# Kernel tuning notes

Measured on AMD Instinct MI355X. Metric: run time of the kernel, lower is better.

The kernel has to match this reference:

```python
import jax, jax.numpy as jnp
import numpy as np

N_EMBED = 16384
CODE_DIM = 32

def l2norm(t, eps=1e-12):
    return t / jnp.clip(jnp.linalg.norm(t, axis=-1, keepdims=True), eps)

def setup_inputs() -> dict:
    key = jax.random.key(0)
    k1, k2 = jax.random.split(key)
    z = jax.random.normal(k1, (8, 1024, CODE_DIM), dtype=jnp.float32)
    codebook = l2norm(jax.random.normal(k2, (N_EMBED, CODE_DIM), dtype=jnp.float32))
    return {"z": z, "codebook": codebook}

def reference(z, codebook):
    # z: [B, S, D]; codebook: [N, D]
    zn = l2norm(z)
    zf = zn.reshape(-1, zn.shape[-1])  # [B*S, D]
    d = (jnp.sum(zf * zf, axis=1, keepdims=True)
         + jnp.sum(codebook * codebook, axis=1)
         - 2.0 * jnp.einsum('bd,nd->bn', zf, codebook))  # [B*S, N]
    encoding_indices = jnp.argmin(d, axis=1)  # [B*S]
    z_q = codebook[encoding_indices]  # [B*S, D]
    return z_q, encoding_indices
```

## Files before the change

### kernel.cpp

```cpp
#include <hip/hip_runtime.h>
#include <math.h>

#define M_ROWS   8192
#define N_CODES  16384
#define D_DIM    32
#define NTHREADS 256

#define DELTA_MARGIN  8e-5f

#define NCHUNK       16
#define CHUNK_CODES  (N_CODES / NCHUNK)
#define SCAN_SLOTS   256

typedef short bf16x8 __attribute__((ext_vector_type(8)));
typedef float f32x4  __attribute__((ext_vector_type(4)));

__device__ inline unsigned short bf16_rne(float f) {
    unsigned u = __float_as_uint(f);
    unsigned r = u + 0x7FFFu + ((u >> 16) & 1u);
    return (unsigned short)(r >> 16);
}

__device__ inline void pack_pair(float f0, float f1, unsigned& hi, unsigned& lo) {
    unsigned short h0 = bf16_rne(f0), h1 = bf16_rne(f1);
    float r0 = f0 - __uint_as_float((unsigned)h0 << 16);
    float r1 = f1 - __uint_as_float((unsigned)h1 << 16);
    unsigned short l0 = bf16_rne(r0), l1 = bf16_rne(r1);
    hi = (unsigned)h0 | ((unsigned)h1 << 16);
    lo = (unsigned)l0 | ((unsigned)l1 << 16);
}

__device__ inline unsigned sortable_u32(float f) {
    unsigned u = __float_as_uint(f);
    return (u & 0x80000000u) ? ~u : (u | 0x80000000u);
}

__global__ void vq_prep_pack(const float* __restrict__ z,
                             const float* __restrict__ codebook,
                             float* __restrict__ zn, float* __restrict__ zz,
                             float* __restrict__ cc,
                             unsigned* __restrict__ chi, unsigned* __restrict__ clo,
                             unsigned* __restrict__ zhi, unsigned* __restrict__ zlo,
                             int* __restrict__ todo_cnt) {
    int gid  = blockIdx.x * NTHREADS + threadIdx.x;
    int row  = gid >> 2;
    int part = gid & 3;
    if (gid == 0) *todo_cnt = 0;

    if (row < N_CODES) {
        const float4* r4 = reinterpret_cast<const float4*>(codebook + (size_t)row * D_DIM);
        float4 v[8];
#pragma unroll
        for (int h = 0; h < 8; ++h) v[h] = r4[h];
        float s = 0.f;
#pragma unroll
        for (int h = 0; h < 8; ++h) {
            s = fmaf(v[h].x, v[h].x, s);
            s = fmaf(v[h].y, v[h].y, s);
            s = fmaf(v[h].z, v[h].z, s);
            s = fmaf(v[h].w, v[h].w, s);
        }
        if (part == 0) cc[row] = s;
#pragma unroll
        for (int k = 0; k < 2; ++k) {
            int h = part * 2 + k;
            unsigned hi0, lo0, hi1, lo1;
            pack_pair(v[h].x, v[h].y, hi0, lo0);
            pack_pair(v[h].z, v[h].w, hi1, lo1);
            chi[row * 16 + 2 * h]     = hi0;  clo[row * 16 + 2 * h]     = lo0;
            chi[row * 16 + 2 * h + 1] = hi1;  clo[row * 16 + 2 * h + 1] = lo1;
        }
    } else {
        int r = row - N_CODES;
        const float4* r4 = reinterpret_cast<const float4*>(z + (size_t)r * D_DIM);
        float4 v[8];
#pragma unroll
        for (int h = 0; h < 8; ++h) v[h] = r4[h];
        float s = 0.f;
#pragma unroll
        for (int h = 0; h < 8; ++h) {
            s = fmaf(v[h].x, v[h].x, s);
            s = fmaf(v[h].y, v[h].y, s);
            s = fmaf(v[h].z, v[h].z, s);
            s = fmaf(v[h].w, v[h].w, s);
        }
        float norm = sqrtf(s);
        norm = fmaxf(norm, 1e-12f);
        float zs = 0.f;
        float4 w[8];
#pragma unroll
        for (int h = 0; h < 8; ++h) {
            w[h].x = v[h].x / norm;
            w[h].y = v[h].y / norm;
            w[h].z = v[h].z / norm;
            w[h].w = v[h].w / norm;
            zs = fmaf(w[h].x, w[h].x, zs);
            zs = fmaf(w[h].y, w[h].y, zs);
            zs = fmaf(w[h].z, w[h].z, zs);
            zs = fmaf(w[h].w, w[h].w, zs);
        }
        if (part == 0) zz[r] = zs;
        float4* zn4 = reinterpret_cast<float4*>(zn + (size_t)r * D_DIM);
#pragma unroll
        for (int k = 0; k < 2; ++k) {
            int h = part * 2 + k;
            zn4[h] = w[h];
            unsigned hi0, lo0, hi1, lo1;
            pack_pair(w[h].x, w[h].y, hi0, lo0);
            pack_pair(w[h].z, w[h].w, hi1, lo1);
            zhi[r * 16 + 2 * h]     = hi0;  zlo[r * 16 + 2 * h]     = lo0;
            zhi[r * 16 + 2 * h + 1] = hi1;  zlo[r * 16 + 2 * h + 1] = lo1;
        }
    }
}

template <int NS>
__global__ __launch_bounds__(NTHREADS, 4)
void vq_mfma(const unsigned short* __restrict__ zhi,
             const unsigned short* __restrict__ zlo,
             const unsigned short* __restrict__ chi,
             const unsigned short* __restrict__ clo,
             float* __restrict__ pmax1, float* __restrict__ pmax2,
             int* __restrict__ pidx) {
    constexpr int SLICE_CODES = N_CODES / NS;
    constexpr int NPAIR = SLICE_CODES / 32;

    const int tid  = threadIdx.x;
    const int wave = tid >> 6;
    const int lane = tid & 63;
    const int rb    = blockIdx.x & 63;
    const int slice = blockIdx.x >> 6;

    const int row_w = rb * 128 + wave * 32;
    const int l15 = lane & 15;
    const int kg  = lane >> 4;
    const int kc  = kg * 8;

    const bf16x8 a_hi0 = *reinterpret_cast<const bf16x8*>(zhi + (size_t)(row_w + l15) * 32 + kc);
    const bf16x8 a_lo0 = *reinterpret_cast<const bf16x8*>(zlo + (size_t)(row_w + l15) * 32 + kc);
    const bf16x8 a_hi1 = *reinterpret_cast<const bf16x8*>(zhi + (size_t)(row_w + 16 + l15) * 32 + kc);
    const bf16x8 a_lo1 = *reinterpret_cast<const bf16x8*>(zlo + (size_t)(row_w + 16 + l15) * 32 + kc);

    const f32x4 zero4 = {0.f, 0.f, 0.f, 0.f};

    float max1[8], max2[8];
    int   idx1[8];
#pragma unroll
    for (int q = 0; q < 8; ++q) { max1[q] = -3.4e38f; max2[q] = -3.4e38f; idx1[q] = 0x7FFFFFFF; }

    auto argup = [&](const f32x4& accA, const f32x4& accB, int code) {
#pragma unroll
        for (int e = 0; e < 4; ++e) {
            float s0 = accA[e];
            max2[e] = __builtin_amdgcn_fmed3f(s0, max1[e], max2[e]);
            bool gt0 = s0 > max1[e];
            max1[e] = gt0 ? s0 : max1[e];
            idx1[e] = gt0 ? code : idx1[e];

            float s1 = accB[e];
            max2[4 + e] = __builtin_amdgcn_fmed3f(s1, max1[4 + e], max2[4 + e]);
            bool gt1 = s1 > max1[4 + e];
            max1[4 + e] = gt1 ? s1 : max1[4 + e];
            idx1[4 + e] = gt1 ? code : idx1[4 + e];
        }
    };
    auto pair_compute = [&](const bf16x8& b0h, const bf16x8& b0l,
                            const bf16x8& b1h, const bf16x8& b1l, int code) {
        f32x4 a00 = __builtin_amdgcn_mfma_f32_16x16x32_bf16(a_lo0, b0l, zero4, 0, 0, 0);
        f32x4 a01 = __builtin_amdgcn_mfma_f32_16x16x32_bf16(a_lo1, b0l, zero4, 0, 0, 0);
        f32x4 a10 = __builtin_amdgcn_mfma_f32_16x16x32_bf16(a_lo0, b1l, zero4, 0, 0, 0);
        f32x4 a11 = __builtin_amdgcn_mfma_f32_16x16x32_bf16(a_lo1, b1l, zero4, 0, 0, 0);
        a00 = __builtin_amdgcn_mfma_f32_16x16x32_bf16(a_lo0, b0h, a00, 0, 0, 0);
        a01 = __builtin_amdgcn_mfma_f32_16x16x32_bf16(a_lo1, b0h, a01, 0, 0, 0);
        a10 = __builtin_amdgcn_mfma_f32_16x16x32_bf16(a_lo0, b1h, a10, 0, 0, 0);
        a11 = __builtin_amdgcn_mfma_f32_16x16x32_bf16(a_lo1, b1h, a11, 0, 0, 0);
        a00 = __builtin_amdgcn_mfma_f32_16x16x32_bf16(a_hi0, b0l, a00, 0, 0, 0);
        a01 = __builtin_amdgcn_mfma_f32_16x16x32_bf16(a_hi1, b0l, a01, 0, 0, 0);
        a10 = __builtin_amdgcn_mfma_f32_16x16x32_bf16(a_hi0, b1l, a10, 0, 0, 0);
        a11 = __builtin_amdgcn_mfma_f32_16x16x32_bf16(a_hi1, b1l, a11, 0, 0, 0);
        a00 = __builtin_amdgcn_mfma_f32_16x16x32_bf16(a_hi0, b0h, a00, 0, 0, 0);
        a01 = __builtin_amdgcn_mfma_f32_16x16x32_bf16(a_hi1, b0h, a01, 0, 0, 0);
        a10 = __builtin_amdgcn_mfma_f32_16x16x32_bf16(a_hi0, b1h, a10, 0, 0, 0);
        a11 = __builtin_amdgcn_mfma_f32_16x16x32_bf16(a_hi1, b1h, a11, 0, 0, 0);
        argup(a00, a01, code);
        argup(a10, a11, code + 16);
    };

    int code = slice * SLICE_CODES + l15;
    bf16x8 b0h = *reinterpret_cast<const bf16x8*>(chi + (size_t)code * 32 + kc);
    bf16x8 b0l = *reinterpret_cast<const bf16x8*>(clo + (size_t)code * 32 + kc);
    bf16x8 b1h = *reinterpret_cast<const bf16x8*>(chi + (size_t)(code + 16) * 32 + kc);
    bf16x8 b1l = *reinterpret_cast<const bf16x8*>(clo + (size_t)(code + 16) * 32 + kc);

    for (int p = 0; p < NPAIR - 1; ++p) {
        const int ncode = code + 32;
        const bf16x8 nb0h = *reinterpret_cast<const bf16x8*>(chi + (size_t)ncode * 32 + kc);
        const bf16x8 nb0l = *reinterpret_cast<const bf16x8*>(clo + (size_t)ncode * 32 + kc);
        const bf16x8 nb1h = *reinterpret_cast<const bf16x8*>(chi + (size_t)(ncode + 16) * 32 + kc);
        const bf16x8 nb1l = *reinterpret_cast<const bf16x8*>(clo + (size_t)(ncode + 16) * 32 + kc);

        pair_compute(b0h, b0l, b1h, b1l, code);

        b0h = nb0h; b0l = nb0l; b1h = nb1h; b1l = nb1l; code = ncode;
    }
    pair_compute(b0h, b0l, b1h, b1l, code);

#pragma unroll
    for (int q = 0; q < 8; ++q) {
        float m1 = max1[q], m2 = max2[q];
        int   i1 = idx1[q];
#pragma unroll
        for (int off = 1; off < 16; off <<= 1) {
            float o1 = __shfl_xor(m1, off);
            float o2 = __shfl_xor(m2, off);
            int   oi = __shfl_xor(i1, off);
            float nm2 = fmaxf(fminf(m1, o1), fmaxf(m2, o2));
            if (o1 > m1 || (o1 == m1 && oi < i1)) { m1 = o1; i1 = oi; }
            m2 = nm2;
        }
        max1[q] = m1; max2[q] = m2; idx1[q] = i1;
    }
    if (l15 == 0) {
#pragma unroll
        for (int q = 0; q < 8; ++q) {
            const int rt = q >> 2, e = q & 3;
            const int row = row_w + rt * 16 + kg * 4 + e;
            pmax1[slice * M_ROWS + row] = max1[q];
            pmax2[slice * M_ROWS + row] = max2[q];
            pidx [slice * M_ROWS + row] = idx1[q];
        }
    }
}

template <int NS>
__global__ void vq_merge(const float* __restrict__ codebook,
                         const float* __restrict__ pmax1,
                         const float* __restrict__ pmax2,
                         const int* __restrict__ pidx,
                         float* __restrict__ zq, float* __restrict__ idx_out,
                         int* __restrict__ todo_cnt, int* __restrict__ todo,
                         unsigned long long* __restrict__ rbest) {
    const int row = blockIdx.x * NTHREADS + threadIdx.x;
    float m1 = pmax1[row], m2 = pmax2[row];
    int   i1 = pidx[row];
#pragma unroll
    for (int s = 1; s < NS; ++s) {
        float o1 = pmax1[s * M_ROWS + row];
        float o2 = pmax2[s * M_ROWS + row];
        int   oi = pidx [s * M_ROWS + row];
        float nm2 = fmaxf(fminf(m1, o1), fmaxf(m2, o2));
        if (o1 > m1) { m1 = o1; i1 = oi; }
        m2 = nm2;
    }
    if (2.0f * (m1 - m2) > DELTA_MARGIN) {
        idx_out[row] = (float)i1;
        const float4* src = reinterpret_cast<const float4*>(codebook + (size_t)i1 * D_DIM);
        float4* dst = reinterpret_cast<float4*>(zq + (size_t)row * D_DIM);
#pragma unroll
        for (int k = 0; k < 8; ++k) dst[k] = src[k];
    } else {
        rbest[row] = 0xFFFFFFFFFFFFFFFFull;
        int p = atomicAdd(todo_cnt, 1);
        todo[p] = row;
    }
}

__global__ __launch_bounds__(NTHREADS)
void vq_cleanup_scan(const float* __restrict__ zn, const float* __restrict__ zz,
                     const float* __restrict__ codebook, const float* __restrict__ cc,
                     const int* __restrict__ todo_cnt, const int* __restrict__ todo,
                     unsigned long long* __restrict__ rbest) {
    const int n = *todo_cnt;
    const int chunk = blockIdx.x & (NCHUNK - 1);
    const int slot  = blockIdx.x >> 4;
    const int tid   = threadIdx.x;
    const int cbase = chunk * CHUNK_CODES;

    for (int i = slot; i < n; i += SCAN_SLOTS) {
        const int row = todo[i];

        float zr[D_DIM];
#pragma unroll
        for (int d = 0; d < D_DIM; ++d) zr[d] = zn[(size_t)row * D_DIM + d];
        const float zzv = zz[row];

        unsigned long long best = 0xFFFFFFFFFFFFFFFFull;
#pragma unroll
        for (int k = 0; k < CHUNK_CODES / NTHREADS; ++k) {
            const int c = cbase + tid + (k << 8);
            const float4* cb = reinterpret_cast<const float4*>(codebook + (size_t)c * D_DIM);
            float dot = 0.f;
#pragma unroll
            for (int h = 0; h < 8; ++h) {
                float4 v = cb[h];
                dot = fmaf(zr[4 * h + 0], v.x, dot);
                dot = fmaf(zr[4 * h + 1], v.y, dot);
                dot = fmaf(zr[4 * h + 2], v.z, dot);
                dot = fmaf(zr[4 * h + 3], v.w, dot);
            }
            float t = zzv + cc[c];
            float dist = fmaf(-2.f, dot, t);
            unsigned long long key =
                ((unsigned long long)sortable_u32(dist) << 32) | (unsigned)c;
            best = (key < best) ? key : best;
        }

#pragma unroll
        for (int off = 32; off >= 1; off >>= 1) {
            unsigned long long ob = __shfl_xor(best, off);
            best = (ob < best) ? ob : best;
        }
        if ((tid & 63) == 0) {
            atomicMin(&rbest[row], best);
        }
    }
}

__global__ __launch_bounds__(NTHREADS)
void vq_cleanup_final(const float* __restrict__ codebook,
                      const int* __restrict__ todo_cnt, const int* __restrict__ todo,
                      const unsigned long long* __restrict__ rbest,
                      float* __restrict__ zq, float* __restrict__ idx_out) {
    const int n = *todo_cnt;
    for (int i = blockIdx.x * NTHREADS + threadIdx.x; i < n; i += gridDim.x * NTHREADS) {
        const int row = todo[i];
        const int bi = (int)(unsigned)(rbest[row] & 0xFFFFFFFFull);
        idx_out[row] = (float)bi;
        const float4* src = reinterpret_cast<const float4*>(codebook + (size_t)bi * D_DIM);
        float4* dst = reinterpret_cast<float4*>(zq + (size_t)row * D_DIM);
#pragma unroll
        for (int k = 0; k < 8; ++k) dst[k] = src[k];
    }
}

#define R_TILE   32
#define NSLICE_F 4
#define SLICE_CODES_F (N_CODES / NSLICE_F)
#define C_TILE   256
#define N_TILES_F (SLICE_CODES_F / C_TILE)
#define CB_PAD   36

__global__ void vq_prep_basic(const float* __restrict__ z,
                              const float* __restrict__ codebook,
                              float* __restrict__ zn,
                              float* __restrict__ zz,
                              float* __restrict__ cc) {
    int gid = blockIdx.x * NTHREADS + threadIdx.x;
    if (blockIdx.x < 64) {
        const float* row = codebook + (size_t)gid * D_DIM;
        float s = 0.f;
#pragma unroll
        for (int d = 0; d < D_DIM; ++d) s = fmaf(row[d], row[d], s);
        cc[gid] = s;
    } else {
        int r = gid - N_CODES;
        const float* row = z + (size_t)r * D_DIM;
        float s = 0.f;
#pragma unroll
        for (int d = 0; d < D_DIM; ++d) { float v = row[d]; s = fmaf(v, v, s); }
        float norm = sqrtf(s);
        norm = fmaxf(norm, 1e-12f);
        float zs = 0.f;
#pragma unroll
        for (int d = 0; d < D_DIM; ++d) {
            float v = row[d] / norm;
            zn[(size_t)r * D_DIM + d] = v;
            zs = fmaf(v, v, zs);
        }
        zz[r] = zs;
    }
}

__global__ __launch_bounds__(NTHREADS, 4)
void vq_main_basic(const float* __restrict__ zn, const float* __restrict__ zz,
                   const float* __restrict__ codebook, const float* __restrict__ cc,
                   float* __restrict__ pminv, int* __restrict__ pmini) {
    __shared__ float cb_lds[C_TILE * CB_PAD];
    __shared__ float zt[R_TILE * D_DIM];
    const int tid = threadIdx.x;
    const int rb = blockIdx.x & 255;
    const int slice = blockIdx.x >> 8;
    const int rg = tid >> 6;
    const int cg = tid & 63;
    const int row_base = rb * R_TILE;
    const int code_base = slice * SLICE_CODES_F;
    const int wrow = row_base + rg * 8;
    {
        float4 v = *reinterpret_cast<const float4*>(zn + (size_t)row_base * D_DIM + tid * 4);
        *reinterpret_cast<float4*>(&zt[tid * 4]) = v;
    }
    float zzr[8];
#pragma unroll
    for (int r = 0; r < 8; ++r) zzr[r] = zz[wrow + r];
    float minv[8]; int mini[8];
#pragma unroll
    for (int r = 0; r < 8; ++r) { minv[r] = 3.4e38f; mini[r] = 0; }
    for (int t = 0; t < N_TILES_F; ++t) {
        const int base = code_base + t * C_TILE;
        __syncthreads();
        {
            const float4* src = reinterpret_cast<const float4*>(codebook + (size_t)(base + tid) * D_DIM);
            float* dstf = &cb_lds[tid * CB_PAD];
#pragma unroll
            for (int k = 0; k < 8; ++k) *reinterpret_cast<float4*>(dstf + k * 4) = src[k];
        }
        __syncthreads();
        float acc[8][4];
#pragma unroll
        for (int r = 0; r < 8; ++r)
#pragma unroll
            for (int j = 0; j < 4; ++j) acc[r][j] = 0.f;
#pragma unroll
        for (int dc = 0; dc < 8; ++dc) {
            float4 cb4[4];
#pragma unroll
            for (int j = 0; j < 4; ++j)
                cb4[j] = *reinterpret_cast<const float4*>(&cb_lds[(cg + 64 * j) * CB_PAD + dc * 4]);
#pragma unroll
            for (int r = 0; r < 8; ++r) {
                const float4 zv = *reinterpret_cast<const float4*>(&zt[(rg * 8 + r) * D_DIM + dc * 4]);
#pragma unroll
                for (int j = 0; j < 4; ++j) {
                    float a = acc[r][j];
                    a = fmaf(zv.x, cb4[j].x, a);
                    a = fmaf(zv.y, cb4[j].y, a);
                    a = fmaf(zv.z, cb4[j].z, a);
                    a = fmaf(zv.w, cb4[j].w, a);
                    acc[r][j] = a;
                }
            }
        }
#pragma unroll
        for (int j = 0; j < 4; ++j) {
            const int code = base + cg + 64 * j;
            const float ccj = cc[code];
#pragma unroll
            for (int r = 0; r < 8; ++r) {
                float tsum = zzr[r] + ccj;
                float dist = fmaf(-2.f, acc[r][j], tsum);
                if (dist < minv[r]) { minv[r] = dist; mini[r] = code; }
            }
        }
    }
#pragma unroll
    for (int r = 0; r < 8; ++r) {
        float v = minv[r]; int i = mini[r];
#pragma unroll
        for (int off = 32; off >= 1; off >>= 1) {
            float ov = __shfl_xor(v, off);
            int   oi = __shfl_xor(i, off);
            if (ov < v || (ov == v && oi < i)) { v = ov; i = oi; }
        }
        minv[r] = v; mini[r] = i;
    }
    if (cg == 0) {
#pragma unroll
        for (int r = 0; r < 8; ++r) {
            pminv[slice * M_ROWS + wrow + r] = minv[r];
            pmini[slice * M_ROWS + wrow + r] = mini[r];
        }
    }
}

__global__ void vq_final_basic(const float* __restrict__ codebook,
                               const float* __restrict__ pminv,
                               const int* __restrict__ pmini,
                               float* __restrict__ zq, float* __restrict__ idx_out) {
    int row = blockIdx.x * NTHREADS + threadIdx.x;
    float bv = pminv[row];
    int   bi = pmini[row];
#pragma unroll
    for (int s = 1; s < NSLICE_F; ++s) {
        float v = pminv[s * M_ROWS + row];
        int   i = pmini[s * M_ROWS + row];
        if (v < bv || (v == bv && i < bi)) { bv = v; bi = i; }
    }
    idx_out[row] = (float)bi;
    const float4* src = reinterpret_cast<const float4*>(codebook + (size_t)bi * D_DIM);
    float4* dst = reinterpret_cast<float4*>(zq + (size_t)row * D_DIM);
#pragma unroll
    for (int k = 0; k < 8; ++k) dst[k] = src[k];
}

static size_t ws_needed(int nslice) {
    return 4ull * (N_CODES + M_ROWS + 3ull * (size_t)nslice * M_ROWS) +
           4ull * (4 + M_ROWS) +
           8ull * M_ROWS +
           2ull * (2ull * N_CODES * D_DIM + 2ull * M_ROWS * D_DIM) + 4096;
}

template <int NS>
static void launch_mfma_path(const float* z, const float* codebook,
                             float* zn, float* zq_out, float* idx_out,
                             void* d_ws, hipStream_t stream) {
    float* cc    = (float*)d_ws;
    float* zz    = cc + N_CODES;
    float* pmax1 = zz + M_ROWS;
    float* pmax2 = pmax1 + (size_t)NS * M_ROWS;
    int*   pidx  = (int*)(pmax2 + (size_t)NS * M_ROWS);
    int*   todo_cnt = pidx + (size_t)NS * M_ROWS;
    int*   todo  = todo_cnt + 4;
    unsigned long long* rbest = (unsigned long long*)(todo + M_ROWS);
    unsigned* chi = (unsigned*)(rbest + M_ROWS);
    unsigned* clo = chi + (size_t)N_CODES * D_DIM / 2;
    unsigned* zhi = clo + (size_t)N_CODES * D_DIM / 2;
    unsigned* zlo = zhi + (size_t)M_ROWS * D_DIM / 2;

    vq_prep_pack<<<384, NTHREADS, 0, stream>>>(z, codebook, zn, zz, cc,
                                               chi, clo, zhi, zlo, todo_cnt);
    vq_mfma<NS><<<64 * NS, NTHREADS, 0, stream>>>(
        (const unsigned short*)zhi, (const unsigned short*)zlo,
        (const unsigned short*)chi, (const unsigned short*)clo,
        pmax1, pmax2, pidx);
    vq_merge<NS><<<M_ROWS / NTHREADS, NTHREADS, 0, stream>>>(
        codebook, pmax1, pmax2, pidx, zq_out, idx_out, todo_cnt, todo, rbest);
    vq_cleanup_scan<<<SCAN_SLOTS * NCHUNK, NTHREADS, 0, stream>>>(
        zn, zz, codebook, cc, todo_cnt, todo, rbest);
    vq_cleanup_final<<<32, NTHREADS, 0, stream>>>(
        codebook, todo_cnt, todo, rbest, zq_out, idx_out);
}

extern "C" void kernel_launch(void* const* d_in, const int* in_sizes, int n_in,
                              void* d_out, int out_size, void* d_ws, size_t ws_size,
                              hipStream_t stream) {
    const float* z        = (const float*)d_in[0];
    const float* codebook = (const float*)d_in[1];

    float* out     = (float*)d_out;
    float* zq_out  = out;
    float* idx_out = out + (size_t)M_ROWS * D_DIM;
    float* zn      = zq_out;

    if (ws_size >= ws_needed(16)) {
        launch_mfma_path<16>(z, codebook, zn, zq_out, idx_out, d_ws, stream);
    } else {
        float* cc    = (float*)d_ws;
        float* zz    = cc + N_CODES;
        float* pminv = zz + M_ROWS;
        int*   pmini = (int*)(pminv + (size_t)NSLICE_F * M_ROWS);

        vq_prep_basic<<<96, NTHREADS, 0, stream>>>(z, codebook, zn, zz, cc);
        vq_main_basic<<<256 * NSLICE_F, NTHREADS, 0, stream>>>(zn, zz, codebook, cc,
                                                               pminv, pmini);
        vq_final_basic<<<M_ROWS / NTHREADS, NTHREADS, 0, stream>>>(codebook, pminv,
                                                                   pmini, zq_out, idx_out);
    }
}
```

Before: 65.28 us.

## Fuse cleanup finalisation into scan via last-block counter, double-buffer codebook loads

Removes the separate vq_cleanup_final launch. Each row now has an arrival counter, and the last of the 16 chunk blocks to finish a row writes its index and gathered codebook vector, which saves one kernel launch and its dependency gap. The MFMA inner loop is also restructured into an explicit two-set ping-pong of codebook register loads, to keep loads further ahead of compute. The cost is extra threadfence, syncthreads and atomic work per todo row in the scan kernel, plus more register pressure in the MFMA kernel.

```diff
diff --git a/kernel.cpp b/kernel.cpp
--- a/kernel.cpp
+++ b/kernel.cpp
@@ -186,24 +186,26 @@
         argup(a10, a11, code + 16);
     };
 
-    int code = slice * SLICE_CODES + l15;
-    bf16x8 b0h = *reinterpret_cast<const bf16x8*>(chi + (size_t)code * 32 + kc);
-    bf16x8 b0l = *reinterpret_cast<const bf16x8*>(clo + (size_t)code * 32 + kc);
-    bf16x8 b1h = *reinterpret_cast<const bf16x8*>(chi + (size_t)(code + 16) * 32 + kc);
-    bf16x8 b1l = *reinterpret_cast<const bf16x8*>(clo + (size_t)(code + 16) * 32 + kc);
-
-    for (int p = 0; p < NPAIR - 1; ++p) {
-        const int ncode = code + 32;
-        const bf16x8 nb0h = *reinterpret_cast<const bf16x8*>(chi + (size_t)ncode * 32 + kc);
-        const bf16x8 nb0l = *reinterpret_cast<const bf16x8*>(clo + (size_t)ncode * 32 + kc);
-        const bf16x8 nb1h = *reinterpret_cast<const bf16x8*>(chi + (size_t)(ncode + 16) * 32 + kc);
-        const bf16x8 nb1l = *reinterpret_cast<const bf16x8*>(clo + (size_t)(ncode + 16) * 32 + kc);
-
-        pair_compute(b0h, b0l, b1h, b1l, code);
-
-        b0h = nb0h; b0l = nb0l; b1h = nb1h; b1l = nb1l; code = ncode;
-    }
-    pair_compute(b0h, b0l, b1h, b1l, code);
+    bf16x8 A0h, A0l, A1h, A1l, B0h, B0l, B1h, B1l;
+    auto loadset = [&](bf16x8& h0, bf16x8& l0, bf16x8& h1, bf16x8& l1, int c) {
+        h0 = *reinterpret_cast<const bf16x8*>(chi + (size_t)c * 32 + kc);
+        l0 = *reinterpret_cast<const bf16x8*>(clo + (size_t)c * 32 + kc);
+        h1 = *reinterpret_cast<const bf16x8*>(chi + (size_t)(c + 16) * 32 + kc);
+        l1 = *reinterpret_cast<const bf16x8*>(clo + (size_t)(c + 16) * 32 + kc);
+    };
+
+    int codeA = slice * SLICE_CODES + l15;
+    loadset(A0h, A0l, A1h, A1l, codeA);
+    for (int p = 0; p + 2 < NPAIR; p += 2) {
+        loadset(B0h, B0l, B1h, B1l, codeA + 32);
+        pair_compute(A0h, A0l, A1h, A1l, codeA);
+        loadset(A0h, A0l, A1h, A1l, codeA + 64);
+        pair_compute(B0h, B0l, B1h, B1l, codeA + 32);
+        codeA += 64;
+    }
+    loadset(B0h, B0l, B1h, B1l, codeA + 32);
+    pair_compute(A0h, A0l, A1h, A1l, codeA);
+    pair_compute(B0h, B0l, B1h, B1l, codeA + 32);
 
 #pragma unroll
     for (int q = 0; q < 8; ++q) {
@@ -239,7 +241,8 @@
                          const int* __restrict__ pidx,
                          float* __restrict__ zq, float* __restrict__ idx_out,
                          int* __restrict__ todo_cnt, int* __restrict__ todo,
-                         unsigned long long* __restrict__ rbest) {
+                         unsigned long long* __restrict__ rbest,
+                         int* __restrict__ rdone) {
     const int row = blockIdx.x * NTHREADS + threadIdx.x;
     float m1 = pmax1[row], m2 = pmax2[row];
     int   i1 = pidx[row];
@@ -260,6 +263,7 @@
         for (int k = 0; k < 8; ++k) dst[k] = src[k];
     } else {
         rbest[row] = 0xFFFFFFFFFFFFFFFFull;
+        rdone[row] = 0;
         int p = atomicAdd(todo_cnt, 1);
         todo[p] = row;
     }
@@ -269,7 +273,9 @@
 void vq_cleanup_scan(const float* __restrict__ zn, const float* __restrict__ zz,
                      const float* __restrict__ codebook, const float* __restrict__ cc,
                      const int* __restrict__ todo_cnt, const int* __restrict__ todo,
-                     unsigned long long* __restrict__ rbest) {
+                     unsigned long long* __restrict__ rbest,
+                     int* __restrict__ rdone,
+                     float* __restrict__ zq, float* __restrict__ idx_out) {
     const int n = *todo_cnt;
     const int chunk = blockIdx.x & (NCHUNK - 1);
     const int slot  = blockIdx.x >> 4;
@@ -313,23 +319,21 @@
         if ((tid & 63) == 0) {
             atomicMin(&rbest[row], best);
         }
-    }
-}
-
-__global__ __launch_bounds__(NTHREADS)
-void vq_cleanup_final(const float* __restrict__ codebook,
-                      const int* __restrict__ todo_cnt, const int* __restrict__ todo,
-                      const unsigned long long* __restrict__ rbest,
-                      float* __restrict__ zq, float* __restrict__ idx_out) {
-    const int n = *todo_cnt;
-    for (int i = blockIdx.x * NTHREADS + threadIdx.x; i < n; i += gridDim.x * NTHREADS) {
-        const int row = todo[i];
-        const int bi = (int)(unsigned)(rbest[row] & 0xFFFFFFFFull);
-        idx_out[row] = (float)bi;
-        const float4* src = reinterpret_cast<const float4*>(codebook + (size_t)bi * D_DIM);
-        float4* dst = reinterpret_cast<float4*>(zq + (size_t)row * D_DIM);
-#pragma unroll
-        for (int k = 0; k < 8; ++k) dst[k] = src[k];
+        __threadfence();
+        __syncthreads();
+        if (tid == 0) {
+            int prev = atomicAdd(&rdone[row], 1);
+            if (prev == NCHUNK - 1) {
+                unsigned long long b = atomicAdd(&rbest[row], 0ull);
+                const int bi = (int)(unsigned)(b & 0xFFFFFFFFull);
+                idx_out[row] = (float)bi;
+                const float4* src = reinterpret_cast<const float4*>(codebook + (size_t)bi * D_DIM);
+                float4* dst = reinterpret_cast<float4*>(zq + (size_t)row * D_DIM);
+#pragma unroll
+                for (int k = 0; k < 8; ++k) dst[k] = src[k];
+            }
+        }
+        __syncthreads();
     }
 }
 
@@ -484,7 +488,7 @@
 
 static size_t ws_needed(int nslice) {
     return 4ull * (N_CODES + M_ROWS + 3ull * (size_t)nslice * M_ROWS) +
-           4ull * (4 + M_ROWS) +
+           4ull * (4 + 2ull * M_ROWS) +
            8ull * M_ROWS +
            2ull * (2ull * N_CODES * D_DIM + 2ull * M_ROWS * D_DIM) + 4096;
 }
@@ -501,7 +505,8 @@
     int*   todo_cnt = pidx + (size_t)NS * M_ROWS;
     int*   todo  = todo_cnt + 4;
     unsigned long long* rbest = (unsigned long long*)(todo + M_ROWS);
-    unsigned* chi = (unsigned*)(rbest + M_ROWS);
+    int*   rdone = (int*)(rbest + M_ROWS);
+    unsigned* chi = (unsigned*)(rdone + M_ROWS);
     unsigned* clo = chi + (size_t)N_CODES * D_DIM / 2;
     unsigned* zhi = clo + (size_t)N_CODES * D_DIM / 2;
     unsigned* zlo = zhi + (size_t)M_ROWS * D_DIM / 2;
@@ -513,11 +518,10 @@
         (const unsigned short*)chi, (const unsigned short*)clo,
         pmax1, pmax2, pidx);
     vq_merge<NS><<<M_ROWS / NTHREADS, NTHREADS, 0, stream>>>(
-        codebook, pmax1, pmax2, pidx, zq_out, idx_out, todo_cnt, todo, rbest);
+        codebook, pmax1, pmax2, pidx, zq_out, idx_out, todo_cnt, todo,
+        rbest, rdone);
     vq_cleanup_scan<<<SCAN_SLOTS * NCHUNK, NTHREADS, 0, stream>>>(
-        zn, zz, codebook, cc, todo_cnt, todo, rbest);
-    vq_cleanup_final<<<32, NTHREADS, 0, stream>>>(
-        codebook, todo_cnt, todo, rbest, zq_out, idx_out);
+        zn, zz, codebook, cc, todo_cnt, todo, rbest, rdone, zq_out, idx_out);
 }
 
 extern "C" void kernel_launch(void* const* d_in, const int* in_sizes, int n_in,
```

Measured after the change: 79.60 us. +21.9%, slower.
